# Optimization experiments

Measured on AMD Instinct MI355X. Metric: run time of the kernel, lower is better.

## Reference

```python
import jax, jax.numpy as jnp
import numpy as np

FFT_NORM = "forward"


def _deq_cplx(qp, scale, mn):
    # qp stores (q_int8 + 127) in [0, 254]; dequant: qp*scale + min, last dim = (re, im)
    f = qp.astype(jnp.float32) * scale + mn
    return jax.lax.complex(f[..., 0], f[..., 1])


def setup_inputs() -> dict:
    key = jax.random.key(0)
    ks = jax.random.split(key, 16)
    B, Cin, Cout, H, W = 8, 32, 32, 256, 256
    NxW, NyW = 32, 17            # half-modes of the spectral weight
    r0, r1, r2, r3 = 16, 16, 16, 9  # Tucker ranks
    inp = {
        "x": jax.random.normal(ks[0], (B, Cin, H, W), dtype=jnp.float32),
        "core_scale": jax.random.uniform(ks[1], (), jnp.float32, 0.001, 0.02),
        "core_min": jax.random.normal(ks[2], (), jnp.float32) * 0.1,
        "factor_scales": jax.random.uniform(ks[3], (4,), jnp.float32, 0.001, 0.02),
        "factor_mins": jax.random.normal(ks[4], (4,), jnp.float32) * 0.1,
        "b_scale": jax.random.uniform(ks[5], (), jnp.float32, 0.001, 0.02),
        "b_min": jax.random.normal(ks[6], (), jnp.float32) * 0.1,
        "q_core": jax.random.randint(ks[7], (r0, r1, r2, r3, 2), 0, 255, jnp.int32),
        "q_f0": jax.random.randint(ks[8], (Cin, r0, 2), 0, 255, jnp.int32),
        "q_f1": jax.random.randint(ks[9], (Cout, r1, 2), 0, 255, jnp.int32),
        "q_f2": jax.random.randint(ks[10], (NxW, r2, 2), 0, 255, jnp.int32),
        "q_f3": jax.random.randint(ks[11], (NyW, r3, 2), 0, 255, jnp.int32),
        "q_bias": jax.random.randint(ks[12], (Cout,), 0, 255, jnp.int32),
    }
    return inp


def reference(x, core_scale, core_min, factor_scales, factor_mins, b_scale, b_min,
              q_core, q_f0, q_f1, q_f2, q_f3, q_bias):
    # 1) rFFT over the last two (spatial) dims
    x_fft = jnp.fft.rfftn(x, axes=(-2, -1), norm=FFT_NORM)  # [B, Cin, Nx, Ny_r] c64

    # 2) dequantize Tucker core + factors, reconstruct complex weight via multi_mode_dot
    core = _deq_cplx(q_core, core_scale, core_min)                       # [r0,r1,r2,r3]
    F0 = _deq_cplx(q_f0, factor_scales[0], factor_mins[0])               # [Cin, r0]
    F1 = _deq_cplx(q_f1, factor_scales[1], factor_mins[1])               # [Cout, r1]
    F2 = _deq_cplx(q_f2, factor_scales[2], factor_mins[2])               # [NxW, r2]
    F3 = _deq_cplx(q_f3, factor_scales[3], factor_mins[3])               # [NyW, r3]
    W = jnp.einsum('ijkl,ai,bj,ck,dl->abcd', core, F0, F1, F2, F3)       # [Cin,Cout,NxW,NyW]

    B, Cin, Nx, Ny_r = x_fft.shape
    CinW, Cout, NxW, NyW = W.shape
    assert Cin == CinW

    # 3) centered-slice channel mixing (faithful to the original double loop)
    cx, nx_neg, nx_pos = Nx // 2, NxW // 2, NxW // 2 + NxW % 2
    cy, ny_neg, ny_pos = Ny_r // 2, NyW // 2, NyW // 2 + NyW % 2
    sx = slice(cx - nx_neg, cx + nx_pos)
    sy = slice(cy - ny_neg, cy + ny_pos)
    Wx = slice(0, nx_pos + nx_neg)
    Wy = slice(0, ny_pos + ny_neg)

    mixed = jnp.einsum('bixy,ioxy->boxy', x_fft[:, :, sx, sy], W[:, :, Wx, Wy])
    out_fft = jnp.zeros((B, Cout, Nx, Ny_r), dtype=x_fft.dtype).at[:, :, sx, sy].set(mixed)

    # 4) inverse rFFT back to the original spatial size
    x_out = jnp.fft.irfftn(out_fft, s=x.shape[2:], axes=(-2, -1), norm=FFT_NORM)

    # 5) dequantized bias (real)
    bias = q_bias.astype(jnp.float32) * b_scale + b_min
    return x_out + bias[None, :, None, None]
```

## Files before the change

### kernel.cpp

```cpp
#include <hip/hip_runtime.h>


__device__ __forceinline__ float2 cfma(float2 a, float2 b, float2 c) {
    c.x = fmaf(a.x, b.x, fmaf(-a.y, b.y, c.x));
    c.y = fmaf(a.x, b.y, fmaf(a.y, b.x, c.y));
    return c;
}
__device__ __forceinline__ float2 cmul(float2 a, float2 b) {
    return make_float2(a.x*b.x - a.y*b.y, a.x*b.y + a.y*b.x);
}

__global__ __launch_bounds__(256) void wprep_kernel(
    const int* __restrict__ q_core, const int* __restrict__ q_f3,
    const float* __restrict__ core_scale, const float* __restrict__ core_min,
    const float* __restrict__ f_scales, const float* __restrict__ f_mins,
    float2* __restrict__ CL)
{
    int d = blockIdx.x >> 4, k = blockIdx.x & 15;
    int ij = threadIdx.x;
    float cs = *core_scale, cm = *core_min;
    float s3 = f_scales[3], m3 = f_mins[3];
    const int* qc = q_core + ((ij*16 + k)*9)*2;
    float2 acc = make_float2(0.f, 0.f);
#pragma unroll
    for (int l = 0; l < 9; ++l) {
        int2 q = *(const int2*)(qc + l*2);
        float2 ce = make_float2(q.x*cs + cm, q.y*cs + cm);
        float2 f3 = make_float2(q_f3[(d*9+l)*2]*s3 + m3, q_f3[(d*9+l)*2+1]*s3 + m3);
        acc = cfma(ce, f3, acc);
    }
    CL[(d*16 + k)*256 + ij] = acc;
}

__global__ __launch_bounds__(256) void weights_kernel(
    const float2* __restrict__ CL, const int* __restrict__ q_f0,
    const int* __restrict__ q_f1, const int* __restrict__ q_f2,
    const float* __restrict__ f_scales, const float* __restrict__ f_mins,
    float2* __restrict__ W4)
{
    __shared__ float2 F0s[512], F1s[512];
    __shared__ float2 C2p[16*17];
    __shared__ float2 A2p[16*33];
    int t = threadIdx.x, m = blockIdx.x;
    int c = m / 17, d = m % 17;
    float s0 = f_scales[0], m0 = f_mins[0];
    float s1 = f_scales[1], m1 = f_mins[1];
    float s2 = f_scales[2], m2 = f_mins[2];

    for (int e = t; e < 512; e += 256) {
        F0s[e] = make_float2(q_f0[2*e]*s0 + m0, q_f0[2*e+1]*s0 + m0);
        F1s[e] = make_float2(q_f1[2*e]*s1 + m1, q_f1[2*e+1]*s1 + m1);
    }
    {
        float2 acc = make_float2(0.f, 0.f);
#pragma unroll
        for (int k = 0; k < 16; ++k) {
            float2 clv = CL[(d*16 + k)*256 + t];
            float2 f2 = make_float2(q_f2[(c*16+k)*2]*s2 + m2,
                                    q_f2[(c*16+k)*2+1]*s2 + m2);
            acc = cfma(clv, f2, acc);
        }
        __syncthreads();
        C2p[(t >> 4)*17 + (t & 15)] = acc;
    }
    __syncthreads();
#pragma unroll
    for (int r = 0; r < 2; ++r) {
        int e = t + r*256; int i = e & 15, b = e >> 4;
        float2 acc = make_float2(0.f, 0.f);
#pragma unroll
        for (int j = 0; j < 16; ++j)
            acc = cfma(C2p[i*17 + j], F1s[b*16 + j], acc);
        A2p[i*33 + b] = acc;
    }
    __syncthreads();
    {
        int b = t & 31, a0 = t >> 5;
#pragma unroll
        for (int q = 0; q < 4; ++q) {
            int a = a0 + 8*q;
            float2 acc = make_float2(0.f, 0.f);
#pragma unroll
            for (int i = 0; i < 16; ++i)
                acc = cfma(F0s[a*16 + i], A2p[i*33 + b], acc);
            W4[m*1024 + a*32 + b] = acc;
        }
    }
}

__global__ __launch_bounds__(256) void fwd_w_kernel(const float* __restrict__ x,
                                                    float2* __restrict__ A1)
{
    __shared__ float ys0[64*65], ys2[64*65], yd02[64*65], yd13[64*65];
    __shared__ float2 twl[17*64];
    int tid = threadIdx.x;
    int row0 = blockIdx.x * 64;

    for (int i = tid; i < 17*64; i += 256) {
        int ki = i >> 6, wp = i & 63;
        int n = ((56 + ki) * wp) & 255;
        float a = n * (1.f/128.f);
        twl[i] = make_float2(cospif(a), -sinpif(a));
    }
    const float2* xf2 = (const float2*)x;
    for (int i2 = tid; i2 < 2048; i2 += 256) {
        int r = i2 >> 5, w2 = i2 & 31;
        const float2* xb = xf2 + (size_t)(row0 + r) * 128 + w2;
        float2 a0 = xb[0], a1 = xb[32], a2 = xb[64], a3 = xb[96];
        int ad = (2*w2)*65 + r;
        float s02 = a0.x + a2.x, s13 = a1.x + a3.x;
        ys0[ad] = s02 + s13;  ys2[ad] = s02 - s13;
        yd02[ad] = a0.x - a2.x;  yd13[ad] = a1.x - a3.x;
        s02 = a0.y + a2.y;  s13 = a1.y + a3.y;
        ys0[ad+65] = s02 + s13;  ys2[ad+65] = s02 - s13;
        yd02[ad+65] = a0.y - a2.y;  yd13[ad+65] = a1.y - a3.y;
    }
    __syncthreads();

    int lane = tid & 63, g = tid >> 6;
    int row = row0 + lane;
    if (g == 0) {
        float2 acc[5] = {};
        for (int wp = 0; wp < 64; ++wp) {
            float y = ys0[wp*65 + lane];
#pragma unroll
            for (int j = 0; j < 5; ++j) {
                float2 t = twl[(4*j)*64 + wp];
                acc[j].x = fmaf(y, t.x, acc[j].x);
                acc[j].y = fmaf(y, t.y, acc[j].y);
            }
        }
#pragma unroll
        for (int j = 0; j < 5; ++j) A1[(4*j)*65536 + row] = acc[j];
    } else if (g == 2) {
        float2 acc[4] = {};
        for (int wp = 0; wp < 64; ++wp) {
            float y = ys2[wp*65 + lane];
#pragma unroll
            for (int j = 0; j < 4; ++j) {
                float2 t = twl[(2+4*j)*64 + wp];
                acc[j].x = fmaf(y, t.x, acc[j].x);
                acc[j].y = fmaf(y, t.y, acc[j].y);
            }
        }
#pragma unroll
        for (int j = 0; j < 4; ++j) A1[(2+4*j)*65536 + row] = acc[j];
    } else if (g == 1) {
        float2 acc[4] = {};
        for (int wp = 0; wp < 64; ++wp) {
            float a = yd02[wp*65 + lane], b = yd13[wp*65 + lane];
#pragma unroll
            for (int j = 0; j < 4; ++j) {
                float2 t = twl[(1+4*j)*64 + wp];
                acc[j].x = fmaf(t.x, a, fmaf( t.y, b, acc[j].x));
                acc[j].y = fmaf(t.y, a, fmaf(-t.x, b, acc[j].y));
            }
        }
#pragma unroll
        for (int j = 0; j < 4; ++j) A1[(1+4*j)*65536 + row] = acc[j];
    } else {
        float2 acc[4] = {};
        for (int wp = 0; wp < 64; ++wp) {
            float a = yd02[wp*65 + lane], b = yd13[wp*65 + lane];
#pragma unroll
            for (int j = 0; j < 4; ++j) {
                float2 t = twl[(3+4*j)*64 + wp];
                acc[j].x = fmaf(t.x, a, fmaf(-t.y, b, acc[j].x));
                acc[j].y = fmaf(t.y, a, fmaf( t.x, b, acc[j].y));
            }
        }
#pragma unroll
        for (int j = 0; j < 4; ++j) A1[(3+4*j)*65536 + row] = acc[j];
    }
}

__global__ __launch_bounds__(256) void fwd_h_kernel(const float2* __restrict__ A1,
                                                    float2* __restrict__ X)
{
    __shared__ float2 tbl[256];
    __shared__ float as_re[8*264];
    __shared__ float as_im[8*264];
    int tid = threadIdx.x;
    int ky = blockIdx.x >> 5, bi0 = (blockIdx.x & 31) * 8;
    tbl[tid] = make_float2(cospif(tid * (1.f/128.f)), -sinpif(tid * (1.f/128.f)));
    for (int idx = tid; idx < 2048; idx += 256) {
        int b = idx >> 8, h = idx & 255;
        float2 v = A1[ky*65536 + (bi0 + b)*256 + h];
        int ad = (h >> 5)*264 + (h & 31)*8 + b;
        as_re[ad] = v.x; as_im[ad] = v.y;
    }
    __syncthreads();
    int lane = tid & 63, g = tid >> 6;
    int bl = lane & 7, q = lane >> 3;
    int kx0 = g * 8;
    float2 acc[8];
#pragma unroll
    for (int j = 0; j < 8; ++j) acc[j] = make_float2(0.f, 0.f);
    int base = q*264 + bl;
    for (int hh = 0; hh < 32; ++hh) {
        float ar = as_re[base + hh*8];
        float ai = as_im[base + hh*8];
#pragma unroll
        for (int j = 0; j < 8; ++j) {
            int kk = kx0 + j + 112;
            float2 t = tbl[(kk * hh) & 255];
            acc[j].x = fmaf(ar, t.x, fmaf(-ai, t.y, acc[j].x));
            acc[j].y = fmaf(ar, t.y, fmaf( ai, t.x, acc[j].y));
        }
    }
    float2 fstep = tbl[q * 32];
    float2 f = make_float2(1.f, 0.f);
#pragma unroll
    for (int j = 0; j < 8; ++j) {
        float2 v = cmul(acc[j], f);
        v.x += __shfl_xor(v.x, 8);  v.y += __shfl_xor(v.y, 8);
        v.x += __shfl_xor(v.x, 16); v.y += __shfl_xor(v.y, 16);
        v.x += __shfl_xor(v.x, 32); v.y += __shfl_xor(v.y, 32);
        acc[j] = v;
        f = cmul(f, fstep);
    }
    if (q == 0) {
        const float inv = 1.f / 65536.f;
#pragma unroll
        for (int j = 0; j < 8; ++j)
            X[((kx0 + j)*17 + ky)*256 + bi0 + bl] =
                make_float2(acc[j].x * inv, acc[j].y * inv);
    }
}

__global__ __launch_bounds__(256) void mix_kernel(const float2* __restrict__ X,
                                                  const float2* __restrict__ W4,
                                                  float2* __restrict__ Mx)
{
    __shared__ float2 Xs[256];
    __shared__ float2 Ws[1024];
    int tid = threadIdx.x, mode = blockIdx.x;
    Xs[tid] = X[mode*256 + tid];
    for (int idx = tid; idx < 1024; idx += 256) Ws[idx] = W4[mode*1024 + idx];
    __syncthreads();
    int b = tid >> 5, o = tid & 31;
    float2 acc = make_float2(0.f, 0.f);
#pragma unroll
    for (int i = 0; i < 32; ++i)
        acc = cfma(Xs[b*32 + i], Ws[i*32 + o], acc);
    Mx[mode*256 + tid] = acc;
}

template<int KY0, int NK>
__device__ __forceinline__ void invh_part(int h, int hh, const float2* ms, float2* Ts)
{
    float2 acc[NK];
#pragma unroll
    for (int j = 0; j < NK; ++j) acc[j] = make_float2(0.f, 0.f);
    int n0 = (112 * h) & 255;
    float tr = cospif(n0 * (1.f/128.f)), ti = sinpif(n0 * (1.f/128.f));
    float sr = cospif(h  * (1.f/128.f)), si = sinpif(h  * (1.f/128.f));
    for (int kx = 0; kx < 32; ++kx) {
#pragma unroll
        for (int j = 0; j < NK; ++j) {
            float2 mv = ms[kx*17 + KY0 + j];
            acc[j].x = fmaf(mv.x, tr, fmaf(-mv.y, ti, acc[j].x));
            acc[j].y = fmaf(mv.x, ti, fmaf( mv.y, tr, acc[j].y));
        }
        float ntr = fmaf(tr, sr, -ti*si);
        ti = fmaf(tr, si, ti*sr);
        tr = ntr;
    }
#pragma unroll
    for (int j = 0; j < NK; ++j) Ts[hh*18 + KY0 + j] = acc[j];
}

__global__ __launch_bounds__(256) void inv_kernel(const float2* __restrict__ Mx,
                                                  const int* __restrict__ q_bias,
                                                  const float* __restrict__ b_scale,
                                                  const float* __restrict__ b_min,
                                                  float* __restrict__ out)
{
    __shared__ float2 ms[544];
    __shared__ __align__(16) float2 Ts[32*18];
    int tid = threadIdx.x;
    int bo = blockIdx.x & 255, hc = blockIdx.x >> 8;
    for (int idx = tid; idx < 544; idx += 256) ms[idx] = Mx[idx*256 + bo];
    __syncthreads();
    {
        int hh = tid & 31, g = tid >> 5;
        int h = hc*32 + hh;
        if (g < 7) {
            switch (g) {
                case 0: invh_part<0, 2>(h, hh, ms, Ts); break;
                case 1: invh_part<2, 2>(h, hh, ms, Ts); break;
                case 2: invh_part<4, 2>(h, hh, ms, Ts); break;
                case 3: invh_part<6, 2>(h, hh, ms, Ts); break;
                case 4: invh_part<8, 2>(h, hh, ms, Ts); break;
                case 5: invh_part<10,2>(h, hh, ms, Ts); break;
                default:invh_part<12,2>(h, hh, ms, Ts); break;
            }
        } else {
            invh_part<14,3>(h, hh, ms, Ts);
        }
    }
    __syncthreads();
    {
        int w0 = tid & 63, hs = tid >> 6;
        float C[17], S[17];
        {
            int n0 = (56 * w0) & 255;
            float tr = cospif(n0 * (1.f/128.f)), ti = sinpif(n0 * (1.f/128.f));
            float sr = cospif(w0 * (1.f/128.f)), si = sinpif(w0 * (1.f/128.f));
#pragma unroll
            for (int ky = 0; ky < 17; ++ky) {
                C[ky] = tr; S[ky] = ti;
                float ntr = fmaf(tr, sr, -ti*si);
                ti = fmaf(tr, si, ti*sr);
                tr = ntr;
            }
        }
        float bias = q_bias[bo & 31] * (*b_scale) + (*b_min);
        float* obase = out + (size_t)bo*65536 + (size_t)hc*32*256;

#pragma unroll
        for (int r = 0; r < 8; ++r) {
            int hh = hs*8 + r;
            const float4* tp = (const float4*)&Ts[hh*18];
            float R0 = 0.f, R1 = 0.f, R2 = 0.f, R3 = 0.f, I1 = 0.f, I3 = 0.f;
#pragma unroll
            for (int kp = 0; kp < 9; ++kp) {
                float vx0, vy0, vx1 = 0.f, vy1 = 0.f;
                if (kp < 8) {
                    float4 v4 = tp[kp];
                    vx0 = v4.x; vy0 = v4.y; vx1 = v4.z; vy1 = v4.w;
                } else {
                    float2 v2 = Ts[hh*18 + 16];
                    vx0 = v2.x; vy0 = v2.y;
                }
#pragma unroll
                for (int half = 0; half < 2; ++half) {
                    if (kp == 8 && half == 1) break;
                    const int ky = 2*kp + half;
                    float vx = half ? vx1 : vx0;
                    float vy = half ? vy1 : vy0;
                    float ur = fmaf(vx, C[ky], -vy*S[ky]);
                    if ((ky & 1) == 0) {
                        if ((ky & 3) == 0) R0 += ur; else R2 += ur;
                    } else {
                        float ui = fmaf(vx, S[ky], vy*C[ky]);
                        if ((ky & 3) == 1) { R1 += ur; I1 += ui; }
                        else               { R3 += ur; I3 += ui; }
                    }
                }
            }
            float e02 = R0 + R2, d02 = R0 - R2;
            float e13 = R1 + R3, di  = I3 - I1;
            float q0 = e02 + e13, q2 = e02 - e13;
            float q1 = d02 + di,  q3 = d02 - di;
            obase[hh*256 + w0]       = fmaf(2.f, q0, bias);
            obase[hh*256 + w0 + 64]  = fmaf(2.f, q1, bias);
            obase[hh*256 + w0 + 128] = fmaf(2.f, q2, bias);
            obase[hh*256 + w0 + 192] = fmaf(2.f, q3, bias);
        }
    }
}

extern "C" void kernel_launch(void* const* d_in, const int* in_sizes, int n_in,
                              void* d_out, int out_size, void* d_ws, size_t ws_size,
                              hipStream_t stream) {
    const float* x          = (const float*)d_in[0];
    const float* core_scale = (const float*)d_in[1];
    const float* core_min   = (const float*)d_in[2];
    const float* f_scales   = (const float*)d_in[3];
    const float* f_mins     = (const float*)d_in[4];
    const float* b_scale    = (const float*)d_in[5];
    const float* b_min      = (const float*)d_in[6];
    const int* q_core = (const int*)d_in[7];
    const int* q_f0   = (const int*)d_in[8];
    const int* q_f1   = (const int*)d_in[9];
    const int* q_f2   = (const int*)d_in[10];
    const int* q_f3   = (const int*)d_in[11];
    const int* q_bias = (const int*)d_in[12];
    float* out = (float*)d_out;

    float2* ws = (float2*)d_ws;
    float2* A1 = ws;
    float2* W4 = ws + 1114112;
    float2* X  = W4 + 557056;
    float2* Mx = X + 139264;
    float2* CL = Mx + 139264;
    (void)ws_size; (void)n_in; (void)in_sizes; (void)out_size;

    wprep_kernel<<<272, 256, 0, stream>>>(q_core, q_f3, core_scale, core_min,
                                          f_scales, f_mins, CL);
    weights_kernel<<<544, 256, 0, stream>>>(CL, q_f0, q_f1, q_f2,
                                            f_scales, f_mins, W4);
    fwd_w_kernel<<<1024, 256, 0, stream>>>(x, A1);
    fwd_h_kernel<<<544, 256, 0, stream>>>(A1, X);
    mix_kernel<<<544, 256, 0, stream>>>(X, W4, Mx);
    inv_kernel<<<2048, 256, 0, stream>>>(Mx, q_bias, b_scale, b_min, out);
}
```

Baseline: 196.0 us.

## Use per-lane twiddles with readlane broadcast and transpose mixed-spectrum layout

The forward W-direction DFT stops building a shared-memory twiddle table. Each lane now computes the twiddles for its own wp index in registers, and they are broadcast inside the loop with readlane, which removes the table setup, a barrier-free LDS read per FMA pair, and shared memory use. Separately, the mix kernel now writes its output transposed (bo-major), so the inverse kernel reads its 544 modes contiguously instead of at a stride of 256. In exchange, the mix kernel's stores become strided, and readlane in an unrolled loop adds SALU/VALU dependency pressure.

```diff
diff --git a/kernel.cpp b/kernel.cpp
--- a/kernel.cpp
+++ b/kernel.cpp
@@ -9,6 +9,7 @@
 __device__ __forceinline__ float2 cmul(float2 a, float2 b) {
     return make_float2(a.x*b.x - a.y*b.y, a.x*b.y + a.y*b.x);
 }
+#define RDL(v, l) __int_as_float(__builtin_amdgcn_readlane(__float_as_int(v), (l)))
 
 __global__ __launch_bounds__(256) void wprep_kernel(
     const int* __restrict__ q_core, const int* __restrict__ q_f3,
@@ -92,16 +93,9 @@
                                                     float2* __restrict__ A1)
 {
     __shared__ float ys0[64*65], ys2[64*65], yd02[64*65], yd13[64*65];
-    __shared__ float2 twl[17*64];
     int tid = threadIdx.x;
     int row0 = blockIdx.x * 64;
 
-    for (int i = tid; i < 17*64; i += 256) {
-        int ki = i >> 6, wp = i & 63;
-        int n = ((56 + ki) * wp) & 255;
-        float a = n * (1.f/128.f);
-        twl[i] = make_float2(cospif(a), -sinpif(a));
-    }
     const float2* xf2 = (const float2*)x;
     for (int i2 = tid; i2 < 2048; i2 += 256) {
         int r = i2 >> 5, w2 = i2 & 31;
@@ -120,53 +114,83 @@
     int lane = tid & 63, g = tid >> 6;
     int row = row0 + lane;
     if (g == 0) {
+        float tjx[5], tjy[5];
+#pragma unroll
+        for (int j = 0; j < 5; ++j) {
+            int n = ((56 + 4*j) * lane) & 255;
+            float a = n * (1.f/128.f);
+            tjx[j] = cospif(a); tjy[j] = -sinpif(a);
+        }
         float2 acc[5] = {};
+#pragma unroll 4
         for (int wp = 0; wp < 64; ++wp) {
             float y = ys0[wp*65 + lane];
 #pragma unroll
             for (int j = 0; j < 5; ++j) {
-                float2 t = twl[(4*j)*64 + wp];
-                acc[j].x = fmaf(y, t.x, acc[j].x);
-                acc[j].y = fmaf(y, t.y, acc[j].y);
+                acc[j].x = fmaf(y, RDL(tjx[j], wp), acc[j].x);
+                acc[j].y = fmaf(y, RDL(tjy[j], wp), acc[j].y);
             }
         }
 #pragma unroll
         for (int j = 0; j < 5; ++j) A1[(4*j)*65536 + row] = acc[j];
     } else if (g == 2) {
+        float tjx[4], tjy[4];
+#pragma unroll
+        for (int j = 0; j < 4; ++j) {
+            int n = ((58 + 4*j) * lane) & 255;
+            float a = n * (1.f/128.f);
+            tjx[j] = cospif(a); tjy[j] = -sinpif(a);
+        }
         float2 acc[4] = {};
+#pragma unroll 4
         for (int wp = 0; wp < 64; ++wp) {
             float y = ys2[wp*65 + lane];
 #pragma unroll
             for (int j = 0; j < 4; ++j) {
-                float2 t = twl[(2+4*j)*64 + wp];
-                acc[j].x = fmaf(y, t.x, acc[j].x);
-                acc[j].y = fmaf(y, t.y, acc[j].y);
+                acc[j].x = fmaf(y, RDL(tjx[j], wp), acc[j].x);
+                acc[j].y = fmaf(y, RDL(tjy[j], wp), acc[j].y);
             }
         }
 #pragma unroll
         for (int j = 0; j < 4; ++j) A1[(2+4*j)*65536 + row] = acc[j];
     } else if (g == 1) {
+        float tjx[4], tjy[4];
+#pragma unroll
+        for (int j = 0; j < 4; ++j) {
+            int n = ((57 + 4*j) * lane) & 255;
+            float a = n * (1.f/128.f);
+            tjx[j] = cospif(a); tjy[j] = -sinpif(a);
+        }
         float2 acc[4] = {};
+#pragma unroll 4
         for (int wp = 0; wp < 64; ++wp) {
             float a = yd02[wp*65 + lane], b = yd13[wp*65 + lane];
 #pragma unroll
             for (int j = 0; j < 4; ++j) {
-                float2 t = twl[(1+4*j)*64 + wp];
-                acc[j].x = fmaf(t.x, a, fmaf( t.y, b, acc[j].x));
-                acc[j].y = fmaf(t.y, a, fmaf(-t.x, b, acc[j].y));
+                float tx = RDL(tjx[j], wp), ty = RDL(tjy[j], wp);
+                acc[j].x = fmaf(tx, a, fmaf( ty, b, acc[j].x));
+                acc[j].y = fmaf(ty, a, fmaf(-tx, b, acc[j].y));
             }
         }
 #pragma unroll
         for (int j = 0; j < 4; ++j) A1[(1+4*j)*65536 + row] = acc[j];
     } else {
+        float tjx[4], tjy[4];
+#pragma unroll
+        for (int j = 0; j < 4; ++j) {
+            int n = ((59 + 4*j) * lane) & 255;
+            float a = n * (1.f/128.f);
+            tjx[j] = cospif(a); tjy[j] = -sinpif(a);
+        }
         float2 acc[4] = {};
+#pragma unroll 4
         for (int wp = 0; wp < 64; ++wp) {
             float a = yd02[wp*65 + lane], b = yd13[wp*65 + lane];
 #pragma unroll
             for (int j = 0; j < 4; ++j) {
-                float2 t = twl[(3+4*j)*64 + wp];
-                acc[j].x = fmaf(t.x, a, fmaf(-t.y, b, acc[j].x));
-                acc[j].y = fmaf(t.y, a, fmaf( t.x, b, acc[j].y));
+                float tx = RDL(tjx[j], wp), ty = RDL(tjy[j], wp);
+                acc[j].x = fmaf(tx, a, fmaf(-ty, b, acc[j].x));
+                acc[j].y = fmaf(ty, a, fmaf( tx, b, acc[j].y));
             }
         }
 #pragma unroll
@@ -243,7 +267,7 @@
 #pragma unroll
     for (int i = 0; i < 32; ++i)
         acc = cfma(Xs[b*32 + i], Ws[i*32 + o], acc);
-    Mx[mode*256 + tid] = acc;
+    Mx[tid*544 + mode] = acc;
 }
 
 template<int KY0, int NK>
@@ -280,7 +304,7 @@
     __shared__ __align__(16) float2 Ts[32*18];
     int tid = threadIdx.x;
     int bo = blockIdx.x & 255, hc = blockIdx.x >> 8;
-    for (int idx = tid; idx < 544; idx += 256) ms[idx] = Mx[idx*256 + bo];
+    for (int idx = tid; idx < 544; idx += 256) ms[idx] = Mx[bo*544 + idx];
     __syncthreads();
     {
         int hh = tid & 31, g = tid >> 5;
```

New measurement: 199.6 us. Within noise of the previous version (+1.8%).
